# Optimization experiments

Hardware: AMD Instinct MI355X
Metric: run time of the kernel (lower is better)

## Reference

```python
import jax, jax.numpy as jnp
import numpy as np

N = 50000      # nodes
E = 800000     # random edges (self-loops appended inside reference)
DIN = 128
DH = 32        # per-head hidden dim of layer 1
H = 8          # heads
DOUT = 32      # output dim (layer 2, concat=False)
NEG_SLOPE = 0.2


def segment_softmax(e, seg, num):
    # numerically stable softmax over variable-size segments (per-destination)
    m = jax.ops.segment_max(e, seg, num_segments=num)
    m = jnp.where(jnp.isfinite(m), m, jnp.zeros_like(m))
    ex = jnp.exp(e - m[seg])
    s = jax.ops.segment_sum(ex, seg, num_segments=num)
    return ex / (s[seg] + 1e-16)


def gatv2_conv(x, src, dst, Wl, Wr, att, bias, heads, dim, concat):
    n = x.shape[0]
    xl = (x @ Wl).reshape(n, heads, dim)   # source transform
    xr = (x @ Wr).reshape(n, heads, dim)   # target transform
    z = xl[src] + xr[dst]                  # [E, H, D] gather per edge
    z = jnp.where(z > 0, z, NEG_SLOPE * z) # LeakyReLU BEFORE attention vector (GATv2)
    e = jnp.einsum('ehd,hd->eh', z, att)   # attention logits [E, H]
    alpha = segment_softmax(e, dst, n)     # softmax over in-edges of each dst
    out = jax.ops.segment_sum(alpha[:, :, None] * xl[src], dst, num_segments=n)
    if concat:
        return out.reshape(n, heads * dim) + bias
    return out.mean(axis=1) + bias


def setup_inputs() -> dict:
    key = jax.random.key(0)
    ks = jax.random.split(key, 12)
    x = jax.random.normal(ks[0], (N, DIN), dtype=jnp.float32)
    edge_index = jax.random.randint(ks[1], (2, E), 0, N, dtype=jnp.int64)
    s = 0.05
    Wl1 = jax.random.normal(ks[2], (DIN, H * DH), dtype=jnp.float32) * s
    Wr1 = jax.random.normal(ks[3], (DIN, H * DH), dtype=jnp.float32) * s
    att1 = jax.random.normal(ks[4], (H, DH), dtype=jnp.float32) * s
    b1 = jnp.zeros((H * DH,), dtype=jnp.float32)
    Wl2 = jax.random.normal(ks[5], (H * DH, H * DOUT), dtype=jnp.float32) * s
    Wr2 = jax.random.normal(ks[6], (H * DH, H * DOUT), dtype=jnp.float32) * s
    att2 = jax.random.normal(ks[7], (H, DOUT), dtype=jnp.float32) * s
    b2 = jnp.zeros((DOUT,), dtype=jnp.float32)
    return {"x": x, "edge_index": edge_index, "Wl1": Wl1, "Wr1": Wr1,
            "att1": att1, "b1": b1, "Wl2": Wl2, "Wr2": Wr2,
            "att2": att2, "b2": b2}


def reference(x, edge_index, Wl1, Wr1, att1, b1, Wl2, Wr2, att2, b2):
    n = x.shape[0]
    loops = jnp.arange(n, dtype=edge_index.dtype)
    src = jnp.concatenate([edge_index[0], loops])  # PyG adds self-loops by default
    dst = jnp.concatenate([edge_index[1], loops])
    h = gatv2_conv(x, src, dst, Wl1, Wr1, att1, b1, H, DH, concat=True)
    h = jax.nn.elu(h)
    out = gatv2_conv(h, src, dst, Wl2, Wr2, att2, b2, H, DOUT, concat=False)
    return out
```

## Files before the change

kernel.cpp:

```cpp
#include <hip/hip_runtime.h>
#include <hip/hip_bf16.h>

typedef __hip_bfloat16 bf16;
typedef __attribute__((ext_vector_type(8))) short bf16x8;
typedef __attribute__((ext_vector_type(4))) float f32x4;

#define N_NODES 50000
#define E_RAW   800000
#define E_TOT   850000
#define H_HEADS 8
#define F_DIM   256
#define NB_SCAN 196

__device__ __forceinline__ float loadF(const void* p, size_t i, int f32) {
    return f32 ? ((const float*)p)[i] : __bfloat162float(((const bf16*)p)[i]);
}
__device__ __forceinline__ int loadI(const void* p, size_t i, int is32) {
    return is32 ? ((const int*)p)[i] : (int)((const long long*)p)[i];
}
__device__ __forceinline__ float uasf(unsigned u) { return __uint_as_float(u); }
__device__ __forceinline__ unsigned f2bfbits(float f) {
    unsigned u = __float_as_uint(f);
    return (u + 0x7fff + ((u >> 16) & 1)) >> 16;
}
__device__ __forceinline__ short f2bfs(float f) {
    unsigned u = __float_as_uint(f);
    return (short)((u + 0x7fff + ((u >> 16) & 1)) >> 16);
}

__global__ void detect_zero(const void* __restrict__ x, const void* __restrict__ ei,
                            int* __restrict__ flags, int* __restrict__ counts) {
    int gid = blockIdx.x * 256 + threadIdx.x;
    if (gid < N_NODES) counts[gid] = 0;
    if (blockIdx.x != 0) return;
    __shared__ int sf[2];
    int t = threadIdx.x;
    if (t < 2) sf[t] = 0;
    __syncthreads();
    const unsigned short* xs = (const unsigned short*)x;
    int f32 = 0;
    for (int i = t; i < 8192; i += 256) {
        unsigned e = (xs[i] >> 7) & 0xFF;
        if (e >= 134) f32 = 1;
    }
    const int* eii = (const int*)ei;
    int odd = 0;
    for (int i = t; i < 1024; i += 256)
        if (eii[2 * i + 1] != 0) odd = 1;
    if (f32) atomicOr(&sf[0], 1);
    if (odd) atomicOr(&sf[1], 1);
    __syncthreads();
    if (t < 2) flags[t] = sf[t];
}

__global__ void prep(const void* __restrict__ wl1, const void* __restrict__ wr1,
                     const void* __restrict__ wl2, const void* __restrict__ wr2,
                     const void* __restrict__ ei,
                     bf16* __restrict__ wb, int* __restrict__ counts,
                     unsigned short* __restrict__ rank,
                     const int* __restrict__ flags) {
    const int f32 = flags[0], is32 = flags[1];
    int gid = blockIdx.x * 256 + threadIdx.x;
    if (gid < E_TOT) {
        int d = (gid < E_RAW) ? loadI(ei, (size_t)E_RAW + gid, is32) : (gid - E_RAW);
        rank[gid] = (unsigned short)atomicAdd(&counts[d], 1);
    }
    for (size_t j = gid; j < 196608; j += (size_t)gridDim.x * 256) {
        const void* src; size_t off, base;
        int k, n;
        if (j < 65536) {
            int half = j >= 32768;
            off = j - (size_t)half * 32768;
            src = half ? wr1 : wl1;
            k = (int)(off >> 8); n = half * 256 + (int)(off & 255);
            base = 0;
        } else {
            size_t jj = j - 65536;
            int half = jj >= 65536;
            off = jj - (size_t)half * 65536;
            src = half ? wr2 : wl2;
            k = (int)(off >> 8); n = half * 256 + (int)(off & 255);
            base = 65536;
        }
        int kb = k >> 5, jo = k & 7;
        int lane = ((k >> 3) & 3) * 16 + (n & 15);
        int ctg = n >> 4;
        size_t dst = base + (((size_t)(kb * 32 + ctg) * 64 + lane) * 8 + jo);
        wb[dst] = __float2bfloat16(loadF(src, off, f32));
    }
}

__global__ void scan1(const int* __restrict__ counts, int* __restrict__ rp,
                      int* __restrict__ bsum) {
    __shared__ int sm[256];
    int b = blockIdx.x, t = threadIdx.x;
    int i = b * 256 + t;
    int v = (i < N_NODES) ? counts[i] : 0;
    sm[t] = v; __syncthreads();
    for (int off = 1; off < 256; off <<= 1) {
        int u = (t >= off) ? sm[t - off] : 0;
        __syncthreads();
        sm[t] += u;
        __syncthreads();
    }
    int incl = sm[t];
    if (i < N_NODES) rp[i] = incl - v;
    if (t == 255) bsum[b] = incl;
}

__global__ void scan2(int* __restrict__ bsum) {
    __shared__ int sm[256];
    int t = threadIdx.x;
    int v = (t < NB_SCAN) ? bsum[t] : 0;
    sm[t] = v; __syncthreads();
    for (int off = 1; off < 256; off <<= 1) {
        int u = (t >= off) ? sm[t - off] : 0;
        __syncthreads();
        sm[t] += u;
        __syncthreads();
    }
    if (t < NB_SCAN) bsum[t] = sm[t] - v;
}

__global__ void scan3(int* __restrict__ rp, const int* __restrict__ bsum) {
    int b = blockIdx.x, t = threadIdx.x;
    int i = b * 256 + t;
    if (i < N_NODES) rp[i] += bsum[b];
    if (i == 0) rp[N_NODES] = E_TOT;
}

__global__ void fill(const void* __restrict__ ei, const int* __restrict__ rp,
                     const unsigned short* __restrict__ rank,
                     int* __restrict__ srcs, const int* __restrict__ flags) {
    const int is32 = flags[1];
    int e = blockIdx.x * 256 + threadIdx.x;
    if (e >= E_TOT) return;
    int s, d;
    if (e < E_RAW) { s = loadI(ei, e, is32); d = loadI(ei, (size_t)E_RAW + e, is32); }
    else           { s = d = e - E_RAW; }
    srcs[rp[d] + rank[e]] = s;
}

__launch_bounds__(256)
__global__ void gemm_mfma(const void* __restrict__ A, const bf16* __restrict__ Wsw,
                          bf16* __restrict__ Cl, bf16* __restrict__ Cr,
                          int M, int K, int aDyn, const int* __restrict__ flags) {
    const int af32 = aDyn ? flags[0] : 0;
    const int tid = threadIdx.x;
    const int w = tid >> 6, lane = tid & 63, q = lane >> 4, l16 = lane & 15;
    const int bRow = blockIdx.x * 64;
    const int ctgBase = blockIdx.y * 16;
    int rowA = bRow + w * 16 + l16;
    if (rowA >= M) rowA = M - 1;
    const short* Ap  = (const short*)A + (size_t)rowA * K + q * 8;
    const float* Apf = (const float*)A + (size_t)rowA * K + q * 8;
    const short* Wp = (const short*)Wsw;
    const int nkb = K >> 5;
    f32x4 acc[16] = {};
    for (int kb = 0; kb < nkb; ++kb) {
        bf16x8 af;
        if (!af32) {
            af = *(const bf16x8*)(Ap + kb * 32);
        } else {
            float4 a0 = *(const float4*)(Apf + kb * 32);
            float4 a1 = *(const float4*)(Apf + kb * 32 + 4);
            af[0] = f2bfs(a0.x); af[1] = f2bfs(a0.y);
            af[2] = f2bfs(a0.z); af[3] = f2bfs(a0.w);
            af[4] = f2bfs(a1.x); af[5] = f2bfs(a1.y);
            af[6] = f2bfs(a1.z); af[7] = f2bfs(a1.w);
        }
        const short* bb = Wp + ((size_t)(kb * 32 + ctgBase) * 64 + lane) * 8;
#pragma unroll
        for (int ct = 0; ct < 16; ++ct) {
            bf16x8 bfr = *(const bf16x8*)(bb + ct * 512);
            acc[ct] = __builtin_amdgcn_mfma_f32_16x16x32_bf16(bfr, af, acc[ct], 0, 0, 0);
        }
    }
    unsigned short* C = (unsigned short*)(ctgBase ? Cr : Cl);
    int row = bRow + w * 16 + l16;
    if (row < M) {
#pragma unroll
        for (int ct = 0; ct < 16; ++ct) {
            int col = ct * 16 + q * 4;
            uint2 o;
            o.x = f2bfbits(acc[ct][0]) | (f2bfbits(acc[ct][1]) << 16);
            o.y = f2bfbits(acc[ct][2]) | (f2bfbits(acc[ct][3]) << 16);
            *(uint2*)(C + (size_t)row * 256 + col) = o;
        }
    }
}

#define EDGE2(Q, PRED)                                                        \
    {                                                                         \
        float2 X0 = {uasf(Q.x << 16), uasf(Q.x & 0xffff0000u)};               \
        float2 X1 = {uasf(Q.y << 16), uasf(Q.y & 0xffff0000u)};               \
        float2 X2 = {uasf(Q.z << 16), uasf(Q.z & 0xffff0000u)};               \
        float2 X3 = {uasf(Q.w << 16), uasf(Q.w & 0xffff0000u)};               \
        float2 z0 = {X0.x + rv0.x, X0.y + rv0.y};                             \
        float2 z1 = {X1.x + rv1.x, X1.y + rv1.y};                             \
        float2 z2 = {X2.x + rv2.x, X2.y + rv2.y};                             \
        float2 z3 = {X3.x + rv3.x, X3.y + rv3.y};                             \
        z0.x = fmaxf(z0.x, 0.2f * z0.x); z0.y = fmaxf(z0.y, 0.2f * z0.y);     \
        z1.x = fmaxf(z1.x, 0.2f * z1.x); z1.y = fmaxf(z1.y, 0.2f * z1.y);     \
        z2.x = fmaxf(z2.x, 0.2f * z2.x); z2.y = fmaxf(z2.y, 0.2f * z2.y);     \
        z3.x = fmaxf(z3.x, 0.2f * z3.x); z3.y = fmaxf(z3.y, 0.2f * z3.y);     \
        float2 p2 = {z0.x * a0.x, z0.y * a0.y};                               \
        p2.x = fmaf(z1.x, a1.x, p2.x); p2.y = fmaf(z1.y, a1.y, p2.y);         \
        p2.x = fmaf(z2.x, a2.x, p2.x); p2.y = fmaf(z2.y, a2.y, p2.y);         \
        p2.x = fmaf(z3.x, a3.x, p2.x); p2.y = fmaf(z3.y, a3.y, p2.y);         \
        float p = p2.x + p2.y;                                                \
        p += __shfl_xor(p, 1); p += __shfl_xor(p, 2);                         \
        float wv = (PRED) ? __expf(p) : 0.f;                                  \
        den += wv;                                                            \
        n0.x = fmaf(wv, X0.x, n0.x); n0.y = fmaf(wv, X0.y, n0.y);             \
        n1.x = fmaf(wv, X1.x, n1.x); n1.y = fmaf(wv, X1.y, n1.y);             \
        n2.x = fmaf(wv, X2.x, n2.x); n2.y = fmaf(wv, X2.y, n2.y);             \
        n3.x = fmaf(wv, X3.x, n3.x); n3.y = fmaf(wv, X3.y, n3.y);             \
    }
__launch_bounds__(256)
__global__ void fused_attn(const int* __restrict__ rp, const int* __restrict__ srcs,
                           const bf16* __restrict__ xl, const bf16* __restrict__ xr,
                           const void* __restrict__ att, const void* __restrict__ bias,
                           void* __restrict__ outp, int mode,
                           const int* __restrict__ flags) {
    const int f32 = flags[0];
    const int tid = threadIdx.x, wid = tid >> 6, lane = tid & 63;
    const int sub = lane & 31;
    const int d = blockIdx.x * 8 + wid * 2 + (lane >> 5);

    const unsigned short* xru = (const unsigned short*)xr;
    uint4 xv = *(const uint4*)(xru + (size_t)d * 256 + sub * 8);
    float2 rv0 = {uasf(xv.x << 16), uasf(xv.x & 0xffff0000u)};
    float2 rv1 = {uasf(xv.y << 16), uasf(xv.y & 0xffff0000u)};
    float2 rv2 = {uasf(xv.z << 16), uasf(xv.z & 0xffff0000u)};
    float2 rv3 = {uasf(xv.w << 16), uasf(xv.w & 0xffff0000u)};
    float2 a0, a1, a2, a3;
    if (f32) {
        float4 t0 = *(const float4*)((const float*)att + sub * 8);
        float4 t1 = *(const float4*)((const float*)att + sub * 8 + 4);
        a0 = {t0.x, t0.y}; a1 = {t0.z, t0.w}; a2 = {t1.x, t1.y}; a3 = {t1.z, t1.w};
    } else {
        uint4 av = *(const uint4*)((const unsigned short*)att + sub * 8);
        a0 = {uasf(av.x << 16), uasf(av.x & 0xffff0000u)};
        a1 = {uasf(av.y << 16), uasf(av.y & 0xffff0000u)};
        a2 = {uasf(av.z << 16), uasf(av.z & 0xffff0000u)};
        a3 = {uasf(av.w << 16), uasf(av.w & 0xffff0000u)};
    }

    const int start = rp[d], cnt = rp[d + 1] - start;
    const int cnt1 = cnt - 1;
    int mA = __shfl(cnt, 0), mB = __shfl(cnt, 32);
    const int common = mA < mB ? mA : mB;
    const int maxc   = mA > mB ? mA : mB;
    const int* sp = srcs + start;
    const unsigned short* xlu = (const unsigned short*)xl + sub * 8;

    float den = 0.f;
    float2 n0 = {0,0}, n1 = {0,0}, n2 = {0,0}, n3 = {0,0};
    int i = 0;
    for (; i + 1 < common; i += 2) {
        int s0 = sp[i], s1 = sp[i + 1];
        uint4 q0 = *(const uint4*)(xlu + (size_t)s0 * 256);
        uint4 q1 = *(const uint4*)(xlu + (size_t)s1 * 256);
        EDGE2(q0, 1);
        EDGE2(q1, 1);
    }
    for (; i < maxc; ++i) {
        int i0 = i < cnt1 ? i : cnt1;
        int s0 = sp[i0];
        uint4 q0 = *(const uint4*)(xlu + (size_t)s0 * 256);
        EDGE2(q0, i < cnt);
    }
    float rd = 1.f / (den + 1e-16f);
    float v[8] = {n0.x * rd, n0.y * rd, n1.x * rd, n1.y * rd,
                  n2.x * rd, n2.y * rd, n3.x * rd, n3.y * rd};

    if (mode == 1) {
        float b[8];
        if (f32) {
            float4 t0 = *(const float4*)((const float*)bias + sub * 8);
            float4 t1 = *(const float4*)((const float*)bias + sub * 8 + 4);
            b[0]=t0.x; b[1]=t0.y; b[2]=t0.z; b[3]=t0.w;
            b[4]=t1.x; b[5]=t1.y; b[6]=t1.z; b[7]=t1.w;
        } else {
            uint4 bv = *(const uint4*)((const unsigned short*)bias + sub * 8);
            b[0]=uasf(bv.x<<16); b[1]=uasf(bv.x&0xffff0000u);
            b[2]=uasf(bv.y<<16); b[3]=uasf(bv.y&0xffff0000u);
            b[4]=uasf(bv.z<<16); b[5]=uasf(bv.z&0xffff0000u);
            b[6]=uasf(bv.w<<16); b[7]=uasf(bv.w&0xffff0000u);
        }
        uint4 o;
        unsigned oo[4];
#pragma unroll
        for (int k = 0; k < 4; ++k) {
            float u0 = v[2*k]   + b[2*k];
            float u1 = v[2*k+1] + b[2*k+1];
            u0 = u0 > 0.f ? u0 : expm1f(u0);
            u1 = u1 > 0.f ? u1 : expm1f(u1);
            oo[k] = f2bfbits(u0) | (f2bfbits(u1) << 16);
        }
        o.x = oo[0]; o.y = oo[1]; o.z = oo[2]; o.w = oo[3];
        *(uint4*)((unsigned short*)outp + (size_t)d * 256 + sub * 8) = o;
    } else {
#pragma unroll
        for (int k = 0; k < 8; ++k) {
            v[k] += __shfl_xor(v[k], 4);
            v[k] += __shfl_xor(v[k], 8);
            v[k] += __shfl_xor(v[k], 16);
        }
        if (sub < 4) {
            int j = sub * 8;
            float o[8];
#pragma unroll
            for (int k = 0; k < 8; ++k)
                o[k] = v[k] * 0.125f + loadF(bias, j + k, f32);
            if (f32) {
                float4 o0 = {o[0], o[1], o[2], o[3]};
                float4 o1 = {o[4], o[5], o[6], o[7]};
                *(float4*)((float*)outp + (size_t)d * 32 + j)     = o0;
                *(float4*)((float*)outp + (size_t)d * 32 + j + 4) = o1;
            } else {
                uint4 ob;
                ob.x = f2bfbits(o[0]) | (f2bfbits(o[1]) << 16);
                ob.y = f2bfbits(o[2]) | (f2bfbits(o[3]) << 16);
                ob.z = f2bfbits(o[4]) | (f2bfbits(o[5]) << 16);
                ob.w = f2bfbits(o[6]) | (f2bfbits(o[7]) << 16);
                *(uint4*)((unsigned short*)outp + (size_t)d * 32 + j) = ob;
            }
        }
    }
}

extern "C" void kernel_launch(void* const* d_in, const int* in_sizes, int n_in,
                              void* d_out, int out_size, void* d_ws, size_t ws_size,
                              hipStream_t stream) {
    const void* x    = d_in[0];
    const void* ei   = d_in[1];
    const void* Wl1  = d_in[2];
    const void* Wr1  = d_in[3];
    const void* att1 = d_in[4];
    const void* b1   = d_in[5];
    const void* Wl2  = d_in[6];
    const void* Wr2  = d_in[7];
    const void* att2 = d_in[8];
    const void* b2   = d_in[9];

    char* p = (char*)d_ws;
    auto take = [&](size_t bytes) { char* r = p; p += (bytes + 255) & ~(size_t)255; return r; };
    int*  flags  = (int*) take(64 * sizeof(int));
    bf16* wb     = (bf16*)take(196608 * sizeof(bf16));
    bf16* xl     = (bf16*)take((size_t)N_NODES * F_DIM * sizeof(bf16));
    bf16* xr     = (bf16*)take((size_t)N_NODES * F_DIM * sizeof(bf16));
    bf16* h1     = (bf16*)take((size_t)N_NODES * F_DIM * sizeof(bf16));
    int*  rp     = (int*) take((N_NODES + 1) * sizeof(int));
    int*  counts = (int*) take(N_NODES * sizeof(int));
    int*  bsum   = (int*) take(256 * sizeof(int));
    unsigned short* rank = (unsigned short*)take((size_t)E_TOT * sizeof(unsigned short));
    int*  srcs   = (int*) take(((size_t)E_TOT + 64) * sizeof(int));

    bf16* W1sw = wb;
    bf16* W2sw = wb + 65536;

    const int GB = (E_TOT + 255) / 256;

    detect_zero<<<196, 256, 0, stream>>>(x, ei, flags, counts);
    prep<<<GB, 256, 0, stream>>>(Wl1, Wr1, Wl2, Wr2, ei, wb, counts, rank, flags);
    scan1<<<NB_SCAN, 256, 0, stream>>>(counts, rp, bsum);
    scan2<<<1, 256, 0, stream>>>(bsum);
    scan3<<<NB_SCAN, 256, 0, stream>>>(rp, bsum);
    fill<<<GB, 256, 0, stream>>>(ei, rp, rank, srcs, flags);

    dim3 ggrd((N_NODES + 63) / 64, 2);

    gemm_mfma<<<ggrd, 256, 0, stream>>>(x, W1sw, xl, xr, N_NODES, 128, 1, flags);
    fused_attn<<<N_NODES / 8, 256, 0, stream>>>(rp, srcs, xl, xr, att1, b1, h1, 1, flags);

    gemm_mfma<<<ggrd, 256, 0, stream>>>(h1, W2sw, xl, xr, N_NODES, 256, 0, flags);
    fused_attn<<<N_NODES / 8, 256, 0, stream>>>(rp, srcs, xl, xr, att2, b2, d_out, 2, flags);
}
```

Before: 409.9 us.

## Retile GEMM to 2x2 warp 64x64 tiles and unify edge loop predication

The MFMA GEMM moves from 16 rows by 256 columns per warp to 64x64 warp tiles laid out 2x2 in a 128x128 block. Each loaded A and B fragment is now reused across four MFMAs instead of the A fragment being shared across sixteen B loads, which cuts B-weight traffic per output. The grid becomes 4 column blocks of 128 rows. The attention kernel's edge loop also processes two edges at a time up to the larger degree of the two half-warps, with predicated tails, so more loads stay in flight when degrees differ, at the cost of some redundant clamped loads.

```diff
diff --git a/kernel.cpp b/kernel.cpp
--- a/kernel.cpp
+++ b/kernel.cpp
@@ -148,44 +148,58 @@
     const int af32 = aDyn ? flags[0] : 0;
     const int tid = threadIdx.x;
     const int w = tid >> 6, lane = tid & 63, q = lane >> 4, l16 = lane & 15;
-    const int bRow = blockIdx.x * 64;
-    const int ctgBase = blockIdx.y * 16;
-    int rowA = bRow + w * 16 + l16;
-    if (rowA >= M) rowA = M - 1;
-    const short* Ap  = (const short*)A + (size_t)rowA * K + q * 8;
-    const float* Apf = (const float*)A + (size_t)rowA * K + q * 8;
+    const int bRow = blockIdx.x * 128 + (w >> 1) * 64;
+    const int bCol = blockIdx.y * 128 + (w & 1) * 64;
+    const int ctg0 = bCol >> 4;
     const short* Wp = (const short*)Wsw;
     const int nkb = K >> 5;
+    int rows[4];
+#pragma unroll
+    for (int i = 0; i < 4; ++i) {
+        int r = bRow + i * 16 + l16;
+        rows[i] = r < M ? r : M - 1;
+    }
     f32x4 acc[16] = {};
     for (int kb = 0; kb < nkb; ++kb) {
-        bf16x8 af;
-        if (!af32) {
-            af = *(const bf16x8*)(Ap + kb * 32);
-        } else {
-            float4 a0 = *(const float4*)(Apf + kb * 32);
-            float4 a1 = *(const float4*)(Apf + kb * 32 + 4);
-            af[0] = f2bfs(a0.x); af[1] = f2bfs(a0.y);
-            af[2] = f2bfs(a0.z); af[3] = f2bfs(a0.w);
-            af[4] = f2bfs(a1.x); af[5] = f2bfs(a1.y);
-            af[6] = f2bfs(a1.z); af[7] = f2bfs(a1.w);
-        }
-        const short* bb = Wp + ((size_t)(kb * 32 + ctgBase) * 64 + lane) * 8;
-#pragma unroll
-        for (int ct = 0; ct < 16; ++ct) {
-            bf16x8 bfr = *(const bf16x8*)(bb + ct * 512);
-            acc[ct] = __builtin_amdgcn_mfma_f32_16x16x32_bf16(bfr, af, acc[ct], 0, 0, 0);
-        }
-    }
-    unsigned short* C = (unsigned short*)(ctgBase ? Cr : Cl);
-    int row = bRow + w * 16 + l16;
-    if (row < M) {
-#pragma unroll
-        for (int ct = 0; ct < 16; ++ct) {
-            int col = ct * 16 + q * 4;
-            uint2 o;
-            o.x = f2bfbits(acc[ct][0]) | (f2bfbits(acc[ct][1]) << 16);
-            o.y = f2bfbits(acc[ct][2]) | (f2bfbits(acc[ct][3]) << 16);
-            *(uint2*)(C + (size_t)row * 256 + col) = o;
+        bf16x8 a[4], b[4];
+#pragma unroll
+        for (int i = 0; i < 4; ++i) {
+            if (!af32) {
+                a[i] = *(const bf16x8*)((const short*)A + (size_t)rows[i] * K + q * 8 + kb * 32);
+            } else {
+                const float* Apf = (const float*)A + (size_t)rows[i] * K + q * 8 + kb * 32;
+                float4 a0 = *(const float4*)(Apf);
+                float4 a1 = *(const float4*)(Apf + 4);
+                a[i][0] = f2bfs(a0.x); a[i][1] = f2bfs(a0.y);
+                a[i][2] = f2bfs(a0.z); a[i][3] = f2bfs(a0.w);
+                a[i][4] = f2bfs(a1.x); a[i][5] = f2bfs(a1.y);
+                a[i][6] = f2bfs(a1.z); a[i][7] = f2bfs(a1.w);
+            }
+        }
+#pragma unroll
+        for (int j = 0; j < 4; ++j)
+            b[j] = *(const bf16x8*)(Wp + ((size_t)(kb * 32 + ctg0 + j) * 64 + lane) * 8);
+#pragma unroll
+        for (int i = 0; i < 4; ++i)
+#pragma unroll
+            for (int j = 0; j < 4; ++j)
+                acc[i * 4 + j] =
+                    __builtin_amdgcn_mfma_f32_16x16x32_bf16(b[j], a[i], acc[i * 4 + j], 0, 0, 0);
+    }
+    unsigned short* C = (unsigned short*)(bCol < 256 ? Cl : Cr);
+    const int cBase = (bCol < 256 ? bCol : bCol - 256) + q * 4;
+#pragma unroll
+    for (int i = 0; i < 4; ++i) {
+        int row = bRow + i * 16 + l16;
+        if (row < M) {
+#pragma unroll
+            for (int j = 0; j < 4; ++j) {
+                f32x4 v = acc[i * 4 + j];
+                uint2 o;
+                o.x = f2bfbits(v[0]) | (f2bfbits(v[1]) << 16);
+                o.y = f2bfbits(v[2]) | (f2bfbits(v[3]) << 16);
+                *(uint2*)(C + (size_t)row * 256 + cBase + j * 16) = o;
+            }
         }
     }
 }
@@ -250,22 +264,23 @@
     const int start = rp[d], cnt = rp[d + 1] - start;
     const int cnt1 = cnt - 1;
     int mA = __shfl(cnt, 0), mB = __shfl(cnt, 32);
-    const int common = mA < mB ? mA : mB;
-    const int maxc   = mA > mB ? mA : mB;
+    const int maxc = mA > mB ? mA : mB;
     const int* sp = srcs + start;
     const unsigned short* xlu = (const unsigned short*)xl + sub * 8;
 
     float den = 0.f;
     float2 n0 = {0,0}, n1 = {0,0}, n2 = {0,0}, n3 = {0,0};
     int i = 0;
-    for (; i + 1 < common; i += 2) {
-        int s0 = sp[i], s1 = sp[i + 1];
+    for (; i + 1 < maxc; i += 2) {
+        int i0 = i < cnt1 ? i : cnt1;
+        int i1 = i + 1 < cnt1 ? i + 1 : cnt1;
+        int s0 = sp[i0], s1 = sp[i1];
         uint4 q0 = *(const uint4*)(xlu + (size_t)s0 * 256);
         uint4 q1 = *(const uint4*)(xlu + (size_t)s1 * 256);
-        EDGE2(q0, 1);
-        EDGE2(q1, 1);
-    }
-    for (; i < maxc; ++i) {
+        EDGE2(q0, i < cnt);
+        EDGE2(q1, i + 1 < cnt);
+    }
+    if (i < maxc) {
         int i0 = i < cnt1 ? i : cnt1;
         int s0 = sp[i0];
         uint4 q0 = *(const uint4*)(xlu + (size_t)s0 * 256);
@@ -370,7 +385,7 @@
     scan3<<<NB_SCAN, 256, 0, stream>>>(rp, bsum);
     fill<<<GB, 256, 0, stream>>>(ei, rp, rank, srcs, flags);
 
-    dim3 ggrd((N_NODES + 63) / 64, 2);
+    dim3 ggrd((N_NODES + 127) / 128, 4);
 
     gemm_mfma<<<ggrd, 256, 0, stream>>>(x, W1sw, xl, xr, N_NODES, 128, 1, flags);
     fused_attn<<<N_NODES / 8, 256, 0, stream>>>(rp, srcs, xl, xr, att1, b1, h1, 1, flags);
```

Result: faster. 388.2 us (-5.3%).
